# Kernel tuning notes

Hardware: AMD Instinct MI355X
Metric: run time of the kernel (lower is better)

The kernel has to match this reference:

```python
import jax, jax.numpy as jnp
import numpy as np

N = 50000        # num_nodes
E = 200000       # num_edges
NODE_IN = 16
EDGE_IN = 8
H = 128          # hidden_dim (also per-head channels in GATConv)
HEADS = 4
L = 3            # num_layers
EPS = 1e-5
NEG_SLOPE = 0.2  # PyG GATConv default


def layer_norm(x, g, b):
    mu = jnp.mean(x, axis=-1, keepdims=True)
    v = jnp.var(x, axis=-1, keepdims=True)
    return (x - mu) * jax.lax.rsqrt(v + EPS) * g + b


def batch_norm_eval(x, g, b, rm, rv):
    return (x - rm) * jax.lax.rsqrt(rv + EPS) * g + b


def gat_layer(x, src, dst, W, a_src, a_dst, bias):
    # x: [N, H] -> per-head features [N, HEADS, H]
    xh = (x @ W).reshape(N, HEADS, H)
    al_src = jnp.sum(xh * a_src, axis=-1)  # [N, HEADS]
    al_dst = jnp.sum(xh * a_dst, axis=-1)  # [N, HEADS]
    alpha = jax.nn.leaky_relu(al_src[src] + al_dst[dst], NEG_SLOPE)  # [E', HEADS]
    # segment softmax over edges grouped by destination node
    m = jax.ops.segment_max(alpha, dst, num_segments=N)
    e = jnp.exp(alpha - m[dst])
    s = jax.ops.segment_sum(e, dst, num_segments=N)
    a = e / (s[dst] + 1e-16)
    msg = xh[src] * a[:, :, None]                 # [E', HEADS, H]
    out = jax.ops.segment_sum(msg, dst, num_segments=N)  # [N, HEADS, H]
    return jnp.mean(out, axis=1) + bias           # concat=False -> head mean


def setup_inputs() -> dict:
    key = jax.random.key(0)
    ks = jax.random.split(key, 24)
    s = 0.1
    inp = {
        "x": jax.random.normal(ks[0], (N, NODE_IN), jnp.float32),
        "edge_index": jax.random.randint(ks[1], (2, E), 0, N, jnp.int32),
        "edge_attr": jax.random.normal(ks[2], (E, EDGE_IN), jnp.float32),
        "shock_mask_nodes": jax.random.randint(ks[3], (N,), 0, 2, jnp.int32),
        # node encoder
        "enc_w": jax.random.normal(ks[4], (NODE_IN + 2, H), jnp.float32) * s,
        "enc_b": jnp.zeros((H,), jnp.float32),
        "enc_ln_g": jnp.ones((H,), jnp.float32),
        "enc_ln_b": jnp.zeros((H,), jnp.float32),
        # GAT layers (stacked over L)
        "gat_w": jax.random.normal(ks[5], (L, H, HEADS * H), jnp.float32) * s,
        "gat_att_src": jax.random.normal(ks[6], (L, HEADS, H), jnp.float32) * s,
        "gat_att_dst": jax.random.normal(ks[7], (L, HEADS, H), jnp.float32) * s,
        "gat_bias": jnp.zeros((L, H), jnp.float32),
        # BatchNorm (eval mode: running stats)
        "bn_g": jnp.ones((L, H), jnp.float32),
        "bn_b": jnp.zeros((L, H), jnp.float32),
        "bn_mean": jax.random.normal(ks[8], (L, H), jnp.float32) * 0.01,
        "bn_var": jnp.ones((L, H), jnp.float32),
        # edge MLP: (2H + EDGE_IN) -> H -> H//2 -> 1
        "em1_w": jax.random.normal(ks[9], (2 * H + EDGE_IN, H), jnp.float32) * s,
        "em1_b": jnp.zeros((H,), jnp.float32),
        "em_ln_g": jnp.ones((H,), jnp.float32),
        "em_ln_b": jnp.zeros((H,), jnp.float32),
        "em2_w": jax.random.normal(ks[10], (H, H // 2), jnp.float32) * s,
        "em2_b": jnp.zeros((H // 2,), jnp.float32),
        "em3_w": jax.random.normal(ks[11], (H // 2, 1), jnp.float32) * s,
        "em3_b": jnp.zeros((1,), jnp.float32),
    }
    return inp


def reference(x, edge_index, edge_attr, shock_mask_nodes,
              enc_w, enc_b, enc_ln_g, enc_ln_b,
              gat_w, gat_att_src, gat_att_dst, gat_bias,
              bn_g, bn_b, bn_mean, bn_var,
              em1_w, em1_b, em_ln_g, em_ln_b,
              em2_w, em2_b, em3_w, em3_b):
    src, dst = edge_index[0], edge_index[1]
    shock = shock_mask_nodes.astype(jnp.float32)[:, None]  # [N,1]
    # downstream indicator: scatter_add shock[src] into tgt, binarize
    down = jax.ops.segment_sum(shock[src, 0], dst, num_segments=N)
    down = (down > 0).astype(jnp.float32)[:, None]
    xa = jnp.concatenate([x, shock, down], axis=1)  # [N, NODE_IN+2]
    # node encoder (dropout off in eval)
    h = jax.nn.relu(layer_norm(xa @ enc_w + enc_b, enc_ln_g, enc_ln_b))
    # add self loops once (PyG GATConv default add_self_loops=True)
    loop = jnp.arange(N, dtype=src.dtype)
    src_sl = jnp.concatenate([src, loop])
    dst_sl = jnp.concatenate([dst, loop])
    for i in range(L):
        h = gat_layer(h, src_sl, dst_sl, gat_w[i], gat_att_src[i], gat_att_dst[i], gat_bias[i])
        h = batch_norm_eval(h, bn_g[i], bn_b[i], bn_mean[i], bn_var[i])
        if i < L - 1:
            h = jax.nn.relu(h)
    # edge predictor (note: source uses raw edge_attr, not augmented)
    edge_input = jnp.concatenate([h[src], h[dst], edge_attr], axis=1)  # [E, 2H+EDGE_IN]
    z = jax.nn.relu(layer_norm(edge_input @ em1_w + em1_b, em_ln_g, em_ln_b))
    z = jax.nn.relu(z @ em2_w + em2_b)
    delta = (z @ em3_w + em3_b)[:, 0]  # [E]
    return delta
```

## Files before the change

### kernel.cpp

```cpp
#include <hip/hip_runtime.h>
#include <hip/hip_bf16.h>


#define N_NODES 50000
#define N_EDGES 200000
#define ETOT    (N_EDGES + N_NODES)
#define HID     128
#define LN_EPS  1e-5f
#define NEG     0.2f
#define NSB     196

typedef __hip_bfloat16 bf16;
typedef __attribute__((ext_vector_type(8))) short v8s;
typedef __attribute__((ext_vector_type(4))) float v4f;
#define MFMA(a, b, c) __builtin_amdgcn_mfma_f32_16x16x32_bf16(a, b, c, 0, 0, 0)

__device__ __forceinline__ float b2f(unsigned short s) {
    return __uint_as_float(((unsigned int)s) << 16);
}
__device__ __forceinline__ unsigned short f2b(float f) {
    __hip_bfloat16 h = __float2bfloat16(f);
    return *reinterpret_cast<unsigned short*>(&h);
}
__device__ __forceinline__ unsigned int pack2(float a, float b) {
    return (unsigned int)f2b(a) | ((unsigned int)f2b(b) << 16);
}
__device__ __forceinline__ float pread(const void* p, size_t i, int isbf) {
    if (isbf) return b2f(((const unsigned short*)p)[i]);
    return ((const float*)p)[i];
}

__global__ void k_fill(float* out, int n, float v) {
    int i = blockIdx.x * blockDim.x + threadIdx.x;
    if (i < n) out[i] = v;
}

__global__ void k_detect(const unsigned short* __restrict__ xbuf,
                         int* __restrict__ flag) {
    int sane = 0;
    for (int j = threadIdx.x; j < 4096; j += 64) {
        unsigned short v = xbuf[2 * j];
        int e = (v >> 7) & 0xFF;
        if (v == 0 || (e > 96 && e < 160)) sane++;
    }
    for (int off = 32; off > 0; off >>= 1) sane += __shfl_down(sane, off);
    if (threadIdx.x == 0) flag[0] = (sane * 10 >= 4096 * 9) ? 1 : 0;
}

struct PrepArgs {
    const void *encw, *encb, *enlg, *enlb, *gatw, *asrc, *adst, *bias,
               *bng, *bnb, *bnm, *bnv, *em1w, *em1b, *emlg, *emlb,
               *em2w, *em2b, *em3w, *em3b;
};
#define PREP_ITEMS (150000 + 8193 + 1024 + 196608 + 32768 + 8192)
__global__ void k_prep(PrepArgs a, float* __restrict__ pool,
                       unsigned short* __restrict__ gwt,
                       unsigned short* __restrict__ uvt,
                       unsigned short* __restrict__ w2t,
                       float* __restrict__ down, int* __restrict__ deg,
                       int* __restrict__ fill, const int* __restrict__ flag) {
    int i = blockIdx.x * 256 + threadIdx.x;
    int bf = flag[0];
    if (i < 150000) {
        int which = i / 50000, idx = i - which * 50000;
        if (which == 0) down[idx] = 0.f;
        else if (which == 1) deg[idx] = 0;
        else fill[idx] = 0;
        return;
    }
    i -= 150000;
    if (i < 8193) {
        const void* s; int off;
        if      (i < 2304) { s = a.encw; off = 0;    }
        else if (i < 2432) { s = a.encb; off = 2304; }
        else if (i < 2560) { s = a.enlg; off = 2432; }
        else if (i < 2688) { s = a.enlb; off = 2560; }
        else if (i < 4224) { s = a.asrc; off = 2688; }
        else if (i < 5760) { s = a.adst; off = 4224; }
        else if (i < 6144) { s = a.bias; off = 5760; }
        else if (i < 6528) { s = a.bng;  off = 6144; }
        else if (i < 6912) { s = a.bnb;  off = 6528; }
        else if (i < 7296) { s = a.bnm;  off = 6912; }
        else if (i < 7680) { s = a.bnv;  off = 7296; }
        else if (i < 7808) { s = a.em1b; off = 7680; }
        else if (i < 7936) { s = a.emlg; off = 7808; }
        else if (i < 8064) { s = a.emlb; off = 7936; }
        else if (i < 8128) { s = a.em2b; off = 8064; }
        else if (i < 8192) { s = a.em3w; off = 8128; }
        else               { s = a.em3b; off = 8192; }
        pool[i] = pread(s, i - off, bf);
        return;
    }
    i -= 8193;
    if (i < 1024) {
        int k = i >> 7, c = i & 127;
        pool[8200 + i] = pread(a.em1w, (size_t)(256 + k) * 128 + c, bf);
        return;
    }
    i -= 1024;
    if (i < 196608) {
        int L = i >> 16, rem = i & 65535, n = rem >> 7, k = rem & 127;
        gwt[i] = f2b(pread(a.gatw, (size_t)L * 65536 + (size_t)k * 512 + n, bf));
        return;
    }
    i -= 196608;
    if (i < 32768) {
        int n = i >> 7, k = i & 127;
        float v = (n < 128) ? pread(a.em1w, (size_t)k * 128 + n, bf)
                            : pread(a.em1w, (size_t)(128 + k) * 128 + (n - 128), bf);
        uvt[i] = f2b(v);
        return;
    }
    i -= 32768;
    if (i < 8192) {
        int n = i >> 7, k = i & 127;
        w2t[i] = f2b(pread(a.em2w, (size_t)k * 64 + n, bf));
    }
}

__global__ void k_graph(const int* __restrict__ ei, const int* __restrict__ shock,
                        float* __restrict__ down, int* __restrict__ deg) {
    int e = blockIdx.x * blockDim.x + threadIdx.x;
    if (e < ETOT) {
        int d = (e < N_EDGES) ? ei[N_EDGES + e] : (e - N_EDGES);
        atomicAdd(&deg[d], 1);
        if (e < N_EDGES && shock[ei[e]] != 0) down[d] = 1.f;
    }
}

__global__ __launch_bounds__(256) void k_scan1(
        const int* __restrict__ deg, int* __restrict__ bsum) {
    __shared__ int red[4];
    int b = blockIdx.x, t = threadIdx.x, lane = t & 63, w = t >> 6;
    int idx = b * 256 + t;
    int v = (idx < N_NODES) ? deg[idx] : 0;
#pragma unroll
    for (int off = 1; off < 64; off <<= 1) v += __shfl_xor(v, off);
    if (lane == 0) red[w] = v;
    __syncthreads();
    if (t == 0) bsum[b] = red[0] + red[1] + red[2] + red[3];
}

__global__ __launch_bounds__(256) void k_scan2(
        const int* __restrict__ deg, const int* __restrict__ bsum,
        int* __restrict__ row_start) {
    __shared__ int red[4];
    __shared__ int wsum[4];
    int b = blockIdx.x, t = threadIdx.x, lane = t & 63, w = t >> 6;
    int pv = (t < b) ? bsum[t] : 0;
    int sm = pv;
#pragma unroll
    for (int off = 1; off < 64; off <<= 1) sm += __shfl_xor(sm, off);
    if (lane == 0) red[w] = sm;
    int idx = b * 256 + t;
    int v = (idx < N_NODES) ? deg[idx] : 0;
    int inc = v;
#pragma unroll
    for (int off = 1; off < 64; off <<= 1) {
        int u = __shfl_up(inc, off);
        if (lane >= off) inc += u;
    }
    if (lane == 63) wsum[w] = inc;
    __syncthreads();
    int boff = red[0] + red[1] + red[2] + red[3];
    int wo = 0;
#pragma unroll
    for (int i = 0; i < 4; i++) if (i < w) wo += wsum[i];
    if (idx < N_NODES) row_start[idx] = boff + wo + (inc - v);
    if (b == 0 && t == 0) row_start[N_NODES] = ETOT;
}

__global__ void k_csr(const int* __restrict__ ei, const int* __restrict__ row_start,
                      int* __restrict__ fill, int* __restrict__ csr_src) {
    int e = blockIdx.x * blockDim.x + threadIdx.x;
    if (e < ETOT) {
        int s, d;
        if (e < N_EDGES) { s = ei[e]; d = ei[N_EDGES + e]; }
        else             { s = e - N_EDGES; d = s; }
        int pos = row_start[d] + atomicAdd(&fill[d], 1);
        csr_src[pos] = s;
    }
}

__global__ __launch_bounds__(256) void k_encoder(
        const void* __restrict__ xraw, const int* __restrict__ flag,
        const int* __restrict__ shock, const float* __restrict__ down,
        const float* __restrict__ enc_w, const float* __restrict__ enc_b,
        const float* __restrict__ ln_g, const float* __restrict__ ln_b,
        unsigned short* __restrict__ h) {
    __shared__ float sw[2304];
    __shared__ float sp[384];
    int t = threadIdx.x;
    for (int i = t; i < 2304; i += 256) sw[i] = enc_w[i];
    if (t < 128)      sp[t] = enc_b[t];
    else if (t < 256) sp[t] = ln_g[t - 128];
    if (t < 128)      sp[256 + t] = ln_b[t];
    __syncthreads();

    int w = t >> 6, l = t & 63;
    int n = blockIdx.x * 4 + w;
    int bf = flag[0];
    int c0 = 2 * l, c1 = c0 + 1;

    float xv = (l < 16) ? pread(xraw, (size_t)n * 16 + l, bf) : 0.f;
    float xs = (float)shock[n];
    float xd = down[n];

    float a0 = sp[c0], a1 = sp[c1];
#pragma unroll
    for (int k = 0; k < 16; k++) {
        float xk = __shfl(xv, k);
        a0 = fmaf(xk, sw[k * HID + c0], a0);
        a1 = fmaf(xk, sw[k * HID + c1], a1);
    }
    a0 = fmaf(xs, sw[16 * HID + c0], a0); a1 = fmaf(xs, sw[16 * HID + c1], a1);
    a0 = fmaf(xd, sw[17 * HID + c0], a0); a1 = fmaf(xd, sw[17 * HID + c1], a1);

    float s = a0 + a1, q = a0 * a0 + a1 * a1;
#pragma unroll
    for (int off = 1; off < 64; off <<= 1) {
        s += __shfl_xor(s, off);
        q += __shfl_xor(q, off);
    }
    float mu = s * (1.f / 128.f);
    float var = q * (1.f / 128.f) - mu * mu;
    float rstd = rsqrtf(var + LN_EPS);
    float v0 = fmaxf((a0 - mu) * rstd * sp[128 + c0] + sp[256 + c0], 0.f);
    float v1 = fmaxf((a1 - mu) * rstd * sp[128 + c1] + sp[256 + c1], 0.f);
    *(unsigned int*)&h[(size_t)n * HID + c0] = pack2(v0, v1);
}

__global__ __launch_bounds__(256, 4) void k_gemm(
        const unsigned short* __restrict__ A, const unsigned short* __restrict__ Wt,
        const float* __restrict__ asrc, const float* __restrict__ adst,
        unsigned short* __restrict__ C,
        float* __restrict__ al_s, float* __restrict__ al_d) {
    __shared__ __align__(16) unsigned short As[64 * 136];
    __shared__ float alp[64][4][2];
    int t = threadIdx.x;
    int lane = t & 63, w = t >> 6, l15 = lane & 15, q = lane >> 4;
    int m0 = blockIdx.x * 64, n0 = blockIdx.y * 128, head = blockIdx.y;
    int c0 = n0 + w * 32 + 2 * l15, c1 = c0 + 1;

    v8s b[2][4];
#pragma unroll
    for (int nt = 0; nt < 2; nt++)
#pragma unroll
        for (int kt = 0; kt < 4; kt++)
            b[nt][kt] = *(const v8s*)&Wt[(size_t)(c0 + nt) * 128 + kt * 32 + q * 8];
#pragma unroll
    for (int it = 0; it < 4; it++) {
        int c = t + it * 256;
        int row = c >> 4, ch = c & 15;
        v8s val = {0, 0, 0, 0, 0, 0, 0, 0};
        if (m0 + row < N_NODES)
            val = *(const v8s*)&A[(size_t)(m0 + row) * 128 + ch * 8];
        *(v8s*)&As[row * 136 + ch * 8] = val;
    }
    __syncthreads();

    v4f acc[4][2] = {};
#pragma unroll
    for (int kt = 0; kt < 4; kt++)
#pragma unroll
        for (int mt = 0; mt < 4; mt++) {
            v8s a = *(const v8s*)&As[(mt * 16 + l15) * 136 + kt * 32 + q * 8];
            acc[mt][0] = MFMA(a, b[0][kt], acc[mt][0]);
            acc[mt][1] = MFMA(a, b[1][kt], acc[mt][1]);
        }
#pragma unroll
    for (int mt = 0; mt < 4; mt++)
#pragma unroll
        for (int r = 0; r < 4; r++) {
            int node = m0 + mt * 16 + q * 4 + r;
            if (node < N_NODES)
                *(unsigned int*)&C[(size_t)node * 512 + c0] =
                    pack2(acc[mt][0][r], acc[mt][1][r]);
        }

    float ps0 = asrc[c0], ps1 = asrc[c1];
    float pd0 = adst[c0], pd1 = adst[c1];
#pragma unroll
    for (int mt = 0; mt < 4; mt++)
#pragma unroll
        for (int r = 0; r < 4; r++) {
            float vs = acc[mt][0][r] * ps0 + acc[mt][1][r] * ps1;
            float vd = acc[mt][0][r] * pd0 + acc[mt][1][r] * pd1;
#pragma unroll
            for (int off = 1; off < 16; off <<= 1) {
                vs += __shfl_xor(vs, off);
                vd += __shfl_xor(vd, off);
            }
            if (l15 == 0) {
                alp[mt * 16 + q * 4 + r][w][0] = vs;
                alp[mt * 16 + q * 4 + r][w][1] = vd;
            }
        }
    __syncthreads();
    if (t < 64) {
        int node = m0 + t;
        if (node < N_NODES) {
            float ss = alp[t][0][0] + alp[t][1][0] + alp[t][2][0] + alp[t][3][0];
            float sd = alp[t][0][1] + alp[t][1][1] + alp[t][2][1] + alp[t][3][1];
            al_s[node * 4 + head] = ss;
            al_d[node * 4 + head] = sd;
        }
    }
}

__global__ __launch_bounds__(256) void k_aggregate(
        const unsigned short* __restrict__ xh, const float* __restrict__ al_src,
        const float* __restrict__ al_dst,
        const int* __restrict__ row_start, const int* __restrict__ csr_src,
        const float* __restrict__ bias,
        const float* __restrict__ bn_g, const float* __restrict__ bn_b,
        const float* __restrict__ bn_m, const float* __restrict__ bn_v,
        unsigned short* __restrict__ h, int relu_flag) {
    int w = threadIdx.x >> 6, l = threadIdx.x & 63;
    int n = blockIdx.x * 4 + w;
    int hh = l >> 4, c8 = l & 15;
    int r0 = row_start[n], r1 = row_start[n + 1];
    float ad = al_dst[n * 4 + hh];
    float sh = 0.f;
    float acc[8] = {};
    for (int j = r0; j < r1; j++) {
        int s = csr_src[j];
        float a = al_src[s * 4 + hh] + ad;
        a = (a >= 0.f) ? a : NEG * a;
        float we = __expf(a);
        sh += we;
        v8s row = *(const v8s*)&xh[(size_t)s * 512 + l * 8];
#pragma unroll
        for (int i = 0; i < 8; i++)
            acc[i] = fmaf(we, b2f((unsigned short)row[i]), acc[i]);
    }
    float inv = 1.f / (sh + 1e-16f);
#pragma unroll
    for (int i = 0; i < 8; i++) {
        acc[i] *= inv;
        acc[i] += __shfl_xor(acc[i], 16);
        acc[i] += __shfl_xor(acc[i], 32);
    }
    if (hh == 0) {
        int cbase = c8 * 8;
        short o[8];
#pragma unroll
        for (int i = 0; i < 8; i++) {
            int c = cbase + i;
            float v = 0.25f * acc[i] + bias[c];
            v = (v - bn_m[c]) * rsqrtf(bn_v[c] + LN_EPS) * bn_g[c] + bn_b[c];
            if (relu_flag) v = fmaxf(v, 0.f);
            o[i] = (short)f2b(v);
        }
        *(v8s*)&h[(size_t)n * 128 + cbase] = *(const v8s*)o;
    }
}

__global__ __launch_bounds__(256, 4) void k_uvgemm(
        const unsigned short* __restrict__ A, const unsigned short* __restrict__ Wt,
        unsigned short* __restrict__ UV) {
    __shared__ __align__(16) unsigned short As[64 * 136];
    int t = threadIdx.x;
    int lane = t & 63, w = t >> 6, l15 = lane & 15, q = lane >> 4;
    int m0 = blockIdx.x * 64, n0 = blockIdx.y * 128;
    int c0 = n0 + w * 32 + 2 * l15;

    v8s b[2][4];
#pragma unroll
    for (int nt = 0; nt < 2; nt++)
#pragma unroll
        for (int kt = 0; kt < 4; kt++)
            b[nt][kt] = *(const v8s*)&Wt[(size_t)(c0 + nt) * 128 + kt * 32 + q * 8];
#pragma unroll
    for (int it = 0; it < 4; it++) {
        int c = t + it * 256;
        int row = c >> 4, ch = c & 15;
        v8s val = {0, 0, 0, 0, 0, 0, 0, 0};
        if (m0 + row < N_NODES)
            val = *(const v8s*)&A[(size_t)(m0 + row) * 128 + ch * 8];
        *(v8s*)&As[row * 136 + ch * 8] = val;
    }
    __syncthreads();

    v4f acc[4][2] = {};
#pragma unroll
    for (int kt = 0; kt < 4; kt++)
#pragma unroll
        for (int mt = 0; mt < 4; mt++) {
            v8s a = *(const v8s*)&As[(mt * 16 + l15) * 136 + kt * 32 + q * 8];
            acc[mt][0] = MFMA(a, b[0][kt], acc[mt][0]);
            acc[mt][1] = MFMA(a, b[1][kt], acc[mt][1]);
        }
#pragma unroll
    for (int mt = 0; mt < 4; mt++)
#pragma unroll
        for (int r = 0; r < 4; r++) {
            int node = m0 + mt * 16 + q * 4 + r;
            if (node < N_NODES)
                *(unsigned int*)&UV[(size_t)node * 256 + c0] =
                    pack2(acc[mt][0][r], acc[mt][1][r]);
        }
}

__global__ __launch_bounds__(256) void k_edgemlp2(
        const unsigned short* __restrict__ UV, const int* __restrict__ ei,
        const void* __restrict__ eraw, const int* __restrict__ flag,
        const float* __restrict__ w1e, const float* __restrict__ em1b,
        const float* __restrict__ lng, const float* __restrict__ lnb,
        const unsigned short* __restrict__ w2t, const float* __restrict__ em2b,
        const float* __restrict__ em3w, const float* __restrict__ em3b,
        float* __restrict__ out) {
    __shared__ __align__(16) unsigned short za[64 * 136];
    __shared__ float w1e_s[1024];
    __shared__ unsigned short ea_s[64 * 8];
    __shared__ int idx_s[128];
    __shared__ float part[4][64];

    int t = threadIdx.x;
    int lane = t & 63, w = t >> 6, l15 = lane & 15, q = lane >> 4;
    int e0 = blockIdx.x * 64;
    int bf = flag[0];

    for (int i = t; i < 1024; i += 256) w1e_s[i] = w1e[i];
    if (t < 64) {
        idx_s[t * 2]     = ei[e0 + t];
        idx_s[t * 2 + 1] = ei[N_EDGES + e0 + t];
        if (bf) {
            *(v8s*)&ea_s[t * 8] =
                *(const v8s*)((const unsigned short*)eraw + (size_t)(e0 + t) * 8);
        } else {
            short tmp[8];
#pragma unroll
            for (int j = 0; j < 8; j++)
                tmp[j] = (short)f2b(((const float*)eraw)[(size_t)(e0 + t) * 8 + j]);
            *(v8s*)&ea_s[t * 8] = *(const v8s*)tmp;
        }
    }
    __syncthreads();

    int c0 = 2 * lane, c1 = c0 + 1;
    float bc0 = em1b[c0], bc1 = em1b[c1];
    float lg0 = lng[c0], lg1 = lng[c1], lb0 = lnb[c0], lb1 = lnb[c1];

    int el0 = w * 16;
    unsigned int u = *(const unsigned int*)&UV[(size_t)idx_s[el0 * 2] * 256 + c0];
    unsigned int v = *(const unsigned int*)&UV[(size_t)idx_s[el0 * 2 + 1] * 256 + 128 + c0];
#pragma unroll 1
    for (int i = 0; i < 16; i++) {
        int el = w * 16 + i;
        unsigned int uc = u, vc = v;
        if (i < 15) {
            int el2 = el + 1;
            u = *(const unsigned int*)&UV[(size_t)idx_s[el2 * 2] * 256 + c0];
            v = *(const unsigned int*)&UV[(size_t)idx_s[el2 * 2 + 1] * 256 + 128 + c0];
        }
        float e0t = 0.f, e1t = 0.f;
#pragma unroll
        for (int k = 0; k < 8; k++) {
            float eak = b2f(ea_s[el * 8 + k]);
            e0t = fmaf(eak, w1e_s[k * 128 + c0], e0t);
            e1t = fmaf(eak, w1e_s[k * 128 + c1], e1t);
        }
        float z0 = b2f(uc & 0xffff) + b2f(vc & 0xffff) + e0t + bc0;
        float z1 = b2f(uc >> 16) + b2f(vc >> 16) + e1t + bc1;
        float s = z0 + z1, qq = z0 * z0 + z1 * z1;
#pragma unroll
        for (int off = 1; off < 64; off <<= 1) {
            s  += __shfl_xor(s, off);
            qq += __shfl_xor(qq, off);
        }
        float mu = s * (1.f / 128.f);
        float var = qq * (1.f / 128.f) - mu * mu;
        float rstd = rsqrtf(var + LN_EPS);
        float y0 = fmaxf((z0 - mu) * rstd * lg0 + lb0, 0.f);
        float y1 = fmaxf((z1 - mu) * rstd * lg1 + lb1, 0.f);
        *(unsigned int*)&za[el * 136 + c0] = pack2(y0, y1);
    }
    __syncthreads();

    v8s b2[4];
#pragma unroll
    for (int kt = 0; kt < 4; kt++)
        b2[kt] = *(const v8s*)&w2t[(size_t)(w * 16 + l15) * 128 + kt * 32 + q * 8];
    v4f acc2[4] = {};
#pragma unroll
    for (int kt = 0; kt < 4; kt++)
#pragma unroll
        for (int mt = 0; mt < 4; mt++) {
            v8s a = *(const v8s*)&za[(mt * 16 + l15) * 136 + kt * 32 + q * 8];
            acc2[mt] = MFMA(a, b2[kt], acc2[mt]);
        }

    {
        int col = w * 16 + l15;
        float b2c = em2b[col], w3c = em3w[col];
#pragma unroll
        for (int mt = 0; mt < 4; mt++)
#pragma unroll
            for (int r = 0; r < 4; r++) {
                float vv = fmaxf(acc2[mt][r] + b2c, 0.f) * w3c;
#pragma unroll
                for (int off = 1; off < 16; off <<= 1) vv += __shfl_xor(vv, off);
                if (l15 == 0) part[w][mt * 16 + q * 4 + r] = vv;
            }
    }
    __syncthreads();
    if (t < 64)
        out[e0 + t] = part[0][t] + part[1][t] + part[2][t] + part[3][t]
                    + em3b[0];
}

extern "C" __attribute__((visibility("default")))
void kernel_launch(void* const* d_in, const int* in_sizes, int n_in,
                   void* d_out, int out_size, void* d_ws, size_t ws_size,
                   hipStream_t stream) {
    float* out = (float*)d_out;

    static const int EXP_SIZES[24] = {
        800000, 400000, 1600000, 50000, 2304, 128, 128, 128,
        196608, 1536, 1536, 384, 384, 384, 384, 384,
        33792, 128, 128, 128, 8192, 64, 64, 1};
    bool ok = (n_in == 24) && (out_size == N_EDGES);
    if (ok) for (int i = 0; i < 24; i++) ok = ok && (in_sizes[i] == EXP_SIZES[i]);
    if (!ok) {
        k_fill<<<(out_size + 255) / 256, 256, 0, stream>>>(out, out_size, 4.0f);
        return;
    }
    if (ws_size < (size_t)68000000) {
        k_fill<<<(out_size + 255) / 256, 256, 0, stream>>>(out, out_size, 8.0f);
        return;
    }

    const int* ei    = (const int*)d_in[1];
    const int* shock = (const int*)d_in[3];

    char* ws = (char*)d_ws;
    unsigned short* h_bf  = (unsigned short*)(ws + 0);
    unsigned short* xh    = (unsigned short*)(ws + 12800000);
    unsigned short* UV    = xh;
    float* al_s    = (float*)(ws + 64000000);
    float* al_d    = (float*)(ws + 64800000);
    float* down    = (float*)(ws + 65600000);
    int*   deg     = (int*)  (ws + 65800000);
    int*   row_st  = (int*)  (ws + 66000000);
    int*   fill    = (int*)  (ws + 66200064);
    int*   csr_src = (int*)  (ws + 66400064);
    int*   flag    = (int*)  (ws + 67400064);
    unsigned short* gwt = (unsigned short*)(ws + 67400128);
    unsigned short* uvt = (unsigned short*)(ws + 67793344);
    unsigned short* w2t = (unsigned short*)(ws + 67858880);
    float* pool    = (float*)(ws + 67875264);
    int*   bsum    = (int*)  (ws + 67912160);

    float* cencw = pool + 0;    float* cencb = pool + 2304;
    float* cenlg = pool + 2432; float* cenlb = pool + 2560;
    float* casrc = pool + 2688; float* cadst = pool + 4224;
    float* cbias = pool + 5760; float* cbng  = pool + 6144;
    float* cbnb  = pool + 6528; float* cbnm  = pool + 6912;
    float* cbnv  = pool + 7296; float* cem1b = pool + 7680;
    float* cemlg = pool + 7808; float* cemlb = pool + 7936;
    float* cem2b = pool + 8064; float* cem3w = pool + 8128;
    float* cem3b = pool + 8192;
    float* w1e   = pool + 8200;

    k_detect<<<1, 64, 0, stream>>>((const unsigned short*)d_in[0], flag);

    PrepArgs pa;
    pa.encw = d_in[4];  pa.encb = d_in[5];  pa.enlg = d_in[6];  pa.enlb = d_in[7];
    pa.gatw = d_in[8];  pa.asrc = d_in[9];  pa.adst = d_in[10]; pa.bias = d_in[11];
    pa.bng  = d_in[12]; pa.bnb  = d_in[13]; pa.bnm  = d_in[14]; pa.bnv  = d_in[15];
    pa.em1w = d_in[16]; pa.em1b = d_in[17]; pa.emlg = d_in[18]; pa.emlb = d_in[19];
    pa.em2w = d_in[20]; pa.em2b = d_in[21]; pa.em3w = d_in[22]; pa.em3b = d_in[23];
    k_prep<<<(PREP_ITEMS + 255) / 256, 256, 0, stream>>>(
        pa, pool, gwt, uvt, w2t, down, deg, fill, flag);

    k_graph<<<(ETOT + 255) / 256, 256, 0, stream>>>(ei, shock, down, deg);
    k_scan1<<<NSB, 256, 0, stream>>>(deg, bsum);
    k_scan2<<<NSB, 256, 0, stream>>>(deg, bsum, row_st);
    k_csr<<<(ETOT + 255) / 256, 256, 0, stream>>>(ei, row_st, fill, csr_src);
    k_encoder<<<N_NODES / 4, 256, 0, stream>>>(
        d_in[0], flag, shock, down, cencw, cencb, cenlg, cenlb, h_bf);
    for (int i = 0; i < 3; i++) {
        k_gemm<<<dim3(782, 4), 256, 0, stream>>>(
            h_bf, gwt + (size_t)i * 65536, casrc + i * 512, cadst + i * 512,
            xh, al_s, al_d);
        k_aggregate<<<N_NODES / 4, 256, 0, stream>>>(
            xh, al_s, al_d, row_st, csr_src,
            cbias + i * 128, cbng + i * 128, cbnb + i * 128,
            cbnm + i * 128, cbnv + i * 128, h_bf, (i < 2) ? 1 : 0);
    }
    k_uvgemm<<<dim3(782, 2), 256, 0, stream>>>(h_bf, uvt, UV);
    k_edgemlp2<<<N_EDGES / 64, 256, 0, stream>>>(
        UV, ei, d_in[2], flag, w1e, cem1b, cemlg, cemlb,
        w2t, cem2b, cem3w, cem3b, out);
}
```

Baseline: 484.8 us.

## Vectorize edge MLP first layer per 8 columns and prefetch aggregate rows

The edge-MLP kernel now has 16 lanes cover one edge with 8 columns each, using 16-byte UV loads. The edge-attribute weights are kept transposed as bf16 in registers, and the layernorm reduction shrinks to a 16-lane shuffle. Four edges are processed per wave per iteration instead of one, cutting loop trips and shared-memory weight reads. Separately, the GAT aggregate loop software-prefetches the next neighbor's index, attention score and feature row to hide gather latency. The cost is higher register pressure, and the edge weights are now rounded to bf16.

```diff
diff --git a/kernel.cpp b/kernel.cpp
--- a/kernel.cpp
+++ b/kernel.cpp
@@ -57,6 +57,7 @@
                        unsigned short* __restrict__ gwt,
                        unsigned short* __restrict__ uvt,
                        unsigned short* __restrict__ w2t,
+                       unsigned short* __restrict__ w1et,
                        float* __restrict__ down, int* __restrict__ deg,
                        int* __restrict__ fill, const int* __restrict__ flag) {
     int i = blockIdx.x * 256 + threadIdx.x;
@@ -93,8 +94,8 @@
     }
     i -= 8193;
     if (i < 1024) {
-        int k = i >> 7, c = i & 127;
-        pool[8200 + i] = pread(a.em1w, (size_t)(256 + k) * 128 + c, bf);
+        int c = i >> 3, k = i & 7;
+        w1et[c * 8 + k] = f2b(pread(a.em1w, (size_t)(256 + k) * 128 + c, bf));
         return;
     }
     i -= 1024;
@@ -323,16 +324,22 @@
     float ad = al_dst[n * 4 + hh];
     float sh = 0.f;
     float acc[8] = {};
+    int scur = csr_src[r0];
+    float acur = al_src[scur * 4 + hh];
+    v8s rcur = *(const v8s*)&xh[(size_t)scur * 512 + l * 8];
     for (int j = r0; j < r1; j++) {
-        int s = csr_src[j];
-        float a = al_src[s * 4 + hh] + ad;
+        int jn = (j + 1 < r1) ? j + 1 : j;
+        int snx = csr_src[jn];
+        float anx = al_src[snx * 4 + hh];
+        v8s rnx = *(const v8s*)&xh[(size_t)snx * 512 + l * 8];
+        float a = acur + ad;
         a = (a >= 0.f) ? a : NEG * a;
         float we = __expf(a);
         sh += we;
-        v8s row = *(const v8s*)&xh[(size_t)s * 512 + l * 8];
 #pragma unroll
         for (int i = 0; i < 8; i++)
-            acc[i] = fmaf(we, b2f((unsigned short)row[i]), acc[i]);
+            acc[i] = fmaf(we, b2f((unsigned short)rcur[i]), acc[i]);
+        scur = snx; acur = anx; rcur = rnx;
     }
     float inv = 1.f / (sh + 1e-16f);
 #pragma unroll
@@ -402,17 +409,16 @@
         }
 }
 
-__global__ __launch_bounds__(256) void k_edgemlp2(
+__global__ __launch_bounds__(256) void k_edgemlp3(
         const unsigned short* __restrict__ UV, const int* __restrict__ ei,
         const void* __restrict__ eraw, const int* __restrict__ flag,
-        const float* __restrict__ w1e, const float* __restrict__ em1b,
+        const unsigned short* __restrict__ w1et, const float* __restrict__ em1b,
         const float* __restrict__ lng, const float* __restrict__ lnb,
         const unsigned short* __restrict__ w2t, const float* __restrict__ em2b,
         const float* __restrict__ em3w, const float* __restrict__ em3b,
         float* __restrict__ out) {
     __shared__ __align__(16) unsigned short za[64 * 136];
-    __shared__ float w1e_s[1024];
-    __shared__ unsigned short ea_s[64 * 8];
+    __shared__ __align__(16) unsigned short ea_s[64 * 8];
     __shared__ int idx_s[128];
     __shared__ float part[4][64];
 
@@ -420,8 +426,20 @@
     int lane = t & 63, w = t >> 6, l15 = lane & 15, q = lane >> 4;
     int e0 = blockIdx.x * 64;
     int bf = flag[0];
-
-    for (int i = t; i < 1024; i += 256) w1e_s[i] = w1e[i];
+    int cb = l15 * 8;
+
+    v8s wreg[8];
+#pragma unroll
+    for (int j = 0; j < 8; j++)
+        wreg[j] = *(const v8s*)&w1et[(cb + j) * 8];
+    float bc[8], lg[8], lb[8];
+#pragma unroll
+    for (int j = 0; j < 8; j++) {
+        bc[j] = em1b[cb + j];
+        lg[j] = lng[cb + j];
+        lb[j] = lnb[cb + j];
+    }
+
     if (t < 64) {
         idx_s[t * 2]     = ei[e0 + t];
         idx_s[t * 2 + 1] = ei[N_EDGES + e0 + t];
@@ -438,43 +456,43 @@
     }
     __syncthreads();
 
-    int c0 = 2 * lane, c1 = c0 + 1;
-    float bc0 = em1b[c0], bc1 = em1b[c1];
-    float lg0 = lng[c0], lg1 = lng[c1], lb0 = lnb[c0], lb1 = lnb[c1];
-
-    int el0 = w * 16;
-    unsigned int u = *(const unsigned int*)&UV[(size_t)idx_s[el0 * 2] * 256 + c0];
-    unsigned int v = *(const unsigned int*)&UV[(size_t)idx_s[el0 * 2 + 1] * 256 + 128 + c0];
 #pragma unroll 1
-    for (int i = 0; i < 16; i++) {
-        int el = w * 16 + i;
-        unsigned int uc = u, vc = v;
-        if (i < 15) {
-            int el2 = el + 1;
-            u = *(const unsigned int*)&UV[(size_t)idx_s[el2 * 2] * 256 + c0];
-            v = *(const unsigned int*)&UV[(size_t)idx_s[el2 * 2 + 1] * 256 + 128 + c0];
-        }
-        float e0t = 0.f, e1t = 0.f;
-#pragma unroll
-        for (int k = 0; k < 8; k++) {
-            float eak = b2f(ea_s[el * 8 + k]);
-            e0t = fmaf(eak, w1e_s[k * 128 + c0], e0t);
-            e1t = fmaf(eak, w1e_s[k * 128 + c1], e1t);
-        }
-        float z0 = b2f(uc & 0xffff) + b2f(vc & 0xffff) + e0t + bc0;
-        float z1 = b2f(uc >> 16) + b2f(vc >> 16) + e1t + bc1;
-        float s = z0 + z1, qq = z0 * z0 + z1 * z1;
-#pragma unroll
-        for (int off = 1; off < 64; off <<= 1) {
+    for (int i = 0; i < 4; i++) {
+        int el = w * 16 + i * 4 + q;
+        int src = idx_s[el * 2], dst = idx_s[el * 2 + 1];
+        v8s uu = *(const v8s*)&UV[(size_t)src * 256 + cb];
+        v8s vv = *(const v8s*)&UV[(size_t)dst * 256 + 128 + cb];
+        v8s ea8 = *(const v8s*)&ea_s[el * 8];
+        float eaf[8];
+#pragma unroll
+        for (int k = 0; k < 8; k++) eaf[k] = b2f((unsigned short)ea8[k]);
+        float z[8];
+        float s = 0.f, qq = 0.f;
+#pragma unroll
+        for (int j = 0; j < 8; j++) {
+            float e = 0.f;
+#pragma unroll
+            for (int k = 0; k < 8; k++)
+                e = fmaf(eaf[k], b2f((unsigned short)wreg[j][k]), e);
+            float zz = b2f((unsigned short)uu[j]) + b2f((unsigned short)vv[j])
+                     + e + bc[j];
+            z[j] = zz;
+            s += zz;
+            qq = fmaf(zz, zz, qq);
+        }
+#pragma unroll
+        for (int off = 1; off < 16; off <<= 1) {
             s  += __shfl_xor(s, off);
             qq += __shfl_xor(qq, off);
         }
         float mu = s * (1.f / 128.f);
         float var = qq * (1.f / 128.f) - mu * mu;
         float rstd = rsqrtf(var + LN_EPS);
-        float y0 = fmaxf((z0 - mu) * rstd * lg0 + lb0, 0.f);
-        float y1 = fmaxf((z1 - mu) * rstd * lg1 + lb1, 0.f);
-        *(unsigned int*)&za[el * 136 + c0] = pack2(y0, y1);
+        short o[8];
+#pragma unroll
+        for (int j = 0; j < 8; j++)
+            o[j] = (short)f2b(fmaxf((z[j] - mu) * rstd * lg[j] + lb[j], 0.f));
+        *(v8s*)&za[el * 136 + cb] = *(const v8s*)o;
     }
     __syncthreads();
 
@@ -546,11 +564,12 @@
     int*   fill    = (int*)  (ws + 66200064);
     int*   csr_src = (int*)  (ws + 66400064);
     int*   flag    = (int*)  (ws + 67400064);
-    unsigned short* gwt = (unsigned short*)(ws + 67400128);
-    unsigned short* uvt = (unsigned short*)(ws + 67793344);
-    unsigned short* w2t = (unsigned short*)(ws + 67858880);
-    float* pool    = (float*)(ws + 67875264);
-    int*   bsum    = (int*)  (ws + 67912160);
+    unsigned short* gwt  = (unsigned short*)(ws + 67400128);
+    unsigned short* uvt  = (unsigned short*)(ws + 67793344);
+    unsigned short* w2t  = (unsigned short*)(ws + 67858880);
+    unsigned short* w1et = (unsigned short*)(ws + 67875264);
+    float* pool    = (float*)(ws + 67877312);
+    int*   bsum    = (int*)  (ws + 67910112);
 
     float* cencw = pool + 0;    float* cencb = pool + 2304;
     float* cenlg = pool + 2432; float* cenlb = pool + 2560;
@@ -561,7 +580,6 @@
     float* cemlg = pool + 7808; float* cemlb = pool + 7936;
     float* cem2b = pool + 8064; float* cem3w = pool + 8128;
     float* cem3b = pool + 8192;
-    float* w1e   = pool + 8200;
 
     k_detect<<<1, 64, 0, stream>>>((const unsigned short*)d_in[0], flag);
 
@@ -572,7 +590,7 @@
     pa.em1w = d_in[16]; pa.em1b = d_in[17]; pa.emlg = d_in[18]; pa.emlb = d_in[19];
     pa.em2w = d_in[20]; pa.em2b = d_in[21]; pa.em3w = d_in[22]; pa.em3b = d_in[23];
     k_prep<<<(PREP_ITEMS + 255) / 256, 256, 0, stream>>>(
-        pa, pool, gwt, uvt, w2t, down, deg, fill, flag);
+        pa, pool, gwt, uvt, w2t, w1et, down, deg, fill, flag);
 
     k_graph<<<(ETOT + 255) / 256, 256, 0, stream>>>(ei, shock, down, deg);
     k_scan1<<<NSB, 256, 0, stream>>>(deg, bsum);
@@ -590,7 +608,7 @@
             cbnm + i * 128, cbnv + i * 128, h_bf, (i < 2) ? 1 : 0);
     }
     k_uvgemm<<<dim3(782, 2), 256, 0, stream>>>(h_bf, uvt, UV);
-    k_edgemlp2<<<N_EDGES / 64, 256, 0, stream>>>(
-        UV, ei, d_in[2], flag, w1e, cem1b, cemlg, cemlb,
+    k_edgemlp3<<<N_EDGES / 64, 256, 0, stream>>>(
+        UV, ei, d_in[2], flag, w1et, cem1b, cemlg, cemlb,
         w2t, cem2b, cem3w, cem3b, out);
 }
```

New measurement: 467.0 us. 3.7% less time.
